# Kernel optimization log

Hardware: AMD Instinct MI355X
Metric: run time of the kernel (lower is better)

The kernel has to match this reference:

```python
import jax, jax.numpy as jnp
import numpy as np

B, C, H, W = 4, 256, 64, 64
EPS = 1e-5

def conv1x1(x, w, b):
    # x: [B,Cin,H,W], w: [Cout,Cin], b: [Cout]
    return jnp.einsum('bchw,oc->bohw', x, w) + b[None, :, None, None]

def setup_inputs() -> dict:
    key = jax.random.key(0)
    ks = jax.random.split(key, 16)
    s = 1.0 / np.sqrt(C)
    d = {
        'x1': jax.random.normal(ks[0], (B, C, H, W), jnp.float32),
        'x2': jax.random.normal(ks[1], (B, C, H, W), jnp.float32),
        'q_w': jax.random.normal(ks[2], (C, C), jnp.float32) * s,
        'q_b': jnp.zeros((C,), jnp.float32),
        'k_w': jax.random.normal(ks[3], (C, C), jnp.float32) * s,
        'k_b': jnp.zeros((C,), jnp.float32),
        'v_w': jax.random.normal(ks[4], (C, C), jnp.float32) * s,
        'v_b': jnp.zeros((C,), jnp.float32),
        'proj_w': jax.random.normal(ks[5], (C, C), jnp.float32) * s,
        'proj_b': jnp.zeros((C,), jnp.float32),
        'bn_gamma': jnp.ones((C,), jnp.float32),
        'bn_beta': jnp.zeros((C,), jnp.float32),
        'bn_mean': jax.random.normal(ks[6], (C,), jnp.float32) * 0.1,
        'bn_var': jax.random.uniform(ks[7], (C,), jnp.float32, 0.5, 1.5),
        'gate_w': jax.random.normal(ks[8], (1, 2 * C), jnp.float32) * (1.0 / np.sqrt(2 * C)),
        'gate_b': jnp.zeros((1,), jnp.float32),
    }
    return d

def reference(x1, x2, q_w, q_b, k_w, k_b, v_w, v_b, proj_w, proj_b,
              bn_gamma, bn_beta, bn_mean, bn_var, gate_w, gate_b):
    b, c, h, w = x1.shape
    n = h * w
    scale = c ** (-0.5)
    q = conv1x1(x1, q_w, q_b).reshape(b, c, n)   # [B,C,N]
    k = conv1x1(x2, k_w, k_b).reshape(b, c, n)
    v = conv1x1(x2, v_w, v_b).reshape(b, c, n)
    attn = jnp.einsum('bcn,bcm->bnm', q, k) * scale      # [B,N,N]
    attn = jax.nn.softmax(attn, axis=-1)
    fusion = jnp.einsum('bcm,bnm->bcn', v, attn)          # v @ attn^T
    fusion = fusion.reshape(b, c, h, w)
    # proj: conv1x1 -> BN (eval, running stats) -> ReLU
    fusion = conv1x1(fusion, proj_w, proj_b)
    fusion = (fusion - bn_mean[None, :, None, None]) * (
        bn_gamma[None, :, None, None] * jax.lax.rsqrt(bn_var + EPS)[None, :, None, None]
    ) + bn_beta[None, :, None, None]
    fusion = jax.nn.relu(fusion)
    gate = jax.nn.sigmoid(conv1x1(jnp.concatenate([x1, x2], axis=1), gate_w, gate_b))  # [B,1,H,W]
    return x1 + gate * fusion
```

## Files before the change

### kernel.cpp

```cpp
#include <hip/hip_runtime.h>
#include <hip/hip_bf16.h>

#define NB   4
#define C    256
#define NPIX 4096
#define EPSV 1e-5f
#define K2   0.09016844f
#define MFIX 24.0f
#define KVB  32
#define NSPLIT 4
#define NKVS (NPIX / NSPLIT)
#define NSTEPS (NKVS / KVB)

typedef __bf16 bf16x8 __attribute__((ext_vector_type(8)));
typedef float  f32x4  __attribute__((ext_vector_type(4)));
typedef float  f32x16 __attribute__((ext_vector_type(16)));
typedef unsigned int u32x4 __attribute__((ext_vector_type(4)));
typedef __hip_bfloat16 bf16;

__device__ __forceinline__ void gload16(const void* g, void* l) {
    __builtin_amdgcn_global_load_lds(
        (const __attribute__((address_space(1))) void*)g,
        (__attribute__((address_space(3))) void*)l, 16, 0, 0);
}

__global__ __launch_bounds__(256) void k_transpose(
    const float* __restrict__ x1, const float* __restrict__ x2,
    const float* __restrict__ gate_w,
    const float* __restrict__ qw, const float* __restrict__ kw,
    const float* __restrict__ vw, const float* __restrict__ pw,
    bf16* __restrict__ xt1, bf16* __restrict__ xt2,
    float* __restrict__ gate_ws, bf16* __restrict__ wb)
{
    __shared__ float tile[64][65];
    const int t = threadIdx.x;
    const int z = blockIdx.z;

    if (z == 8) {
        const int sub = blockIdx.x * 4 + blockIdx.y;
        const int i0 = sub * 1024 + t * 4;
        bf16 t4[4];
#pragma unroll
        for (int j = 0; j < 4; ++j) {
            const int i = i0 + j;
            const int p = i >> 16, rem = i & 65535;
            const int o = rem >> 8, cp = rem & 255;
            const int c = cp ^ ((o & 7) << 3);
            const float* w = (p == 0) ? qw : (p == 1) ? kw : (p == 2) ? vw : pw;
            t4[j] = __float2bfloat16(w[o * 256 + c]);
        }
        *reinterpret_cast<uint64_t*>(wb + i0) = *reinterpret_cast<uint64_t*>(t4);
        return;
    }

    const int nt = blockIdx.x, ct = blockIdx.y;
    const int b = z >> 1, which = z & 1;
    const float* x = which ? x2 : x1;
    bf16* xt = which ? xt2 : xt1;
    const int n0 = nt * 64, c0 = ct * 64;

    const float* xp = x + ((size_t)b * C + c0) * NPIX + n0;
#pragma unroll
    for (int i = 0; i < 16; ++i) {
        int cl = (t >> 6) + i * 4, nl = t & 63;
        tile[cl][nl] = xp[(size_t)cl * NPIX + nl];
    }
    __syncthreads();

    {
        int nl = t & 63, qq = t >> 6;
        float s = 0.f;
#pragma unroll
        for (int i = 0; i < 16; ++i) {
            int cl = qq * 16 + i;
            s += tile[cl][nl] * gate_w[which * C + c0 + cl];
        }
        atomicAdd(&gate_ws[b * NPIX + n0 + nl], s);
    }

    bf16* xtp = xt + ((size_t)b * NPIX + n0) * C + c0;
#pragma unroll
    for (int i = 0; i < 16; ++i) {
        int nl = (t >> 6) + i * 4, cl = t & 63;
        xtp[(size_t)nl * C + cl] = __float2bfloat16(tile[cl][nl]);
    }
}

__global__ __launch_bounds__(256) void k_qkv(
    const bf16* __restrict__ xt1, const bf16* __restrict__ xt2,
    const bf16* __restrict__ wb,
    const float* __restrict__ qb, const float* __restrict__ kb,
    const float* __restrict__ vb,
    bf16* __restrict__ Qt, bf16* __restrict__ Kt, bf16* __restrict__ Vv)
{
    __shared__ __align__(16) char wl[32768];
    const int nblk = blockIdx.x, ot = blockIdx.y, zp = blockIdx.z;
    const int b = zp / 3, pidx = zp % 3;
    const bf16* xt = (pidx == 0) ? xt1 : xt2;
    const float* bias = (pidx == 0) ? qb : (pidx == 1) ? kb : vb;
    const int o0 = ot * 64;
    const int t = threadIdx.x;
    const int wave = t >> 6, lane = t & 63;
    const int g = lane >> 4, l15 = lane & 15;

    {
        const char* src = (const char*)(wb + ((size_t)pidx * C + o0) * C);
#pragma unroll
        for (int i = 0; i < 8; ++i) {
            const int L = i * 4096 + t * 16;
            gload16(src + L, wl + L);
        }
    }
    asm volatile("s_waitcnt vmcnt(0)" ::: "memory");
    __syncthreads();

    bf16x8 a[4][8];
#pragma unroll
    for (int ns = 0; ns < 4; ++ns) {
        const bf16* xrow = xt + ((size_t)b * NPIX + nblk * 256 + wave * 64 + ns * 16 + l15) * C;
#pragma unroll
        for (int cb = 0; cb < 8; ++cb)
            a[ns][cb] = *reinterpret_cast<const bf16x8*>(xrow + cb * 32 + 8 * g);
    }

#pragma unroll
    for (int os = 0; os < 4; ++os) {
        const int oo = o0 + os * 16;
        bf16x8 wf[8];
#pragma unroll
        for (int cb = 0; cb < 8; ++cb)
            wf[cb] = *reinterpret_cast<const bf16x8*>(
                wl + (os * 16 + l15) * 512 + ((cb * 64 + 16 * g) ^ ((l15 & 7) << 4)));

        f32x4 acc[4] = {{0,0,0,0},{0,0,0,0},{0,0,0,0},{0,0,0,0}};
#pragma unroll
        for (int cb = 0; cb < 8; ++cb) {
#pragma unroll
            for (int ns = 0; ns < 4; ++ns) {
                if (pidx < 2)
                    acc[ns] = __builtin_amdgcn_mfma_f32_16x16x32_bf16(a[ns][cb], wf[cb], acc[ns], 0, 0, 0);
                else
                    acc[ns] = __builtin_amdgcn_mfma_f32_16x16x32_bf16(wf[cb], a[ns][cb], acc[ns], 0, 0, 0);
            }
        }

        if (pidx < 2) {
            const float bv = bias[oo + l15];
            const float scl = (pidx == 0) ? K2 : 1.0f;
            bf16* Qk = (pidx == 0) ? Qt : Kt;
#pragma unroll
            for (int ns = 0; ns < 4; ++ns) {
                const int n0 = nblk * 256 + wave * 64 + ns * 16;
                bf16* dst = Qk + ((size_t)b * NPIX + n0 + 4 * g) * C + oo + l15;
#pragma unroll
                for (int r = 0; r < 4; ++r)
                    dst[(size_t)r * C] = __float2bfloat16((acc[ns][r] + bv) * scl);
            }
        } else {
#pragma unroll
            for (int ns = 0; ns < 4; ++ns) {
                const int n0 = nblk * 256 + wave * 64 + ns * 16;
                bf16* dst = Vv + ((size_t)b * C + oo + 4 * g) * NPIX + n0 + l15;
#pragma unroll
                for (int r = 0; r < 4; ++r)
                    dst[(size_t)r * NPIX] = __float2bfloat16(acc[ns][r] + bias[oo + 4 * g + r]);
            }
        }
    }
}

#define SMEM_ATTN 65536
#define SZP ((size_t)NPIX * C)

__global__ __launch_bounds__(256, 2) void k_attn(
    const bf16* __restrict__ Qt, const bf16* __restrict__ Kt,
    const bf16* __restrict__ Vv, bf16* __restrict__ O0,
    bf16* __restrict__ O1, float2* __restrict__ mlws)
{
    extern __shared__ __align__(16) char smem[];
    const int id = blockIdx.x;
    const int combo = id & 15, nt = id >> 4;
    const int b = combo >> 2, split = combo & 3;
    const int m_base = split * NKVS;
    const int tid = threadIdx.x;
    const int wave = tid >> 6, lane = tid & 63;
    const int dl = lane & 31, hi = lane >> 5;
    const int n0 = nt * 128 + wave * 32;

    const bf16* Kg = Kt + (size_t)b * NPIX * C;
    const bf16* Vg = Vv + (size_t)b * C * NPIX;

    int o_k[4], o_v[4];
#pragma unroll
    for (int p = 0; p < 4; ++p) {
        const int L = p * 4096 + tid * 16;
        const int kv = L >> 9, colx = L & 511;
        const int col = colx ^ ((kv & 7) << 4);
        o_k[p] = kv * C + (col >> 1);
        const int R = L >> 7, colx2 = L & 127;
        const int col2 = colx2 ^ (((L >> 8) & 7) << 4);
        const int d = 2 * R + (col2 >> 6);
        o_v[p] = d * NPIX + ((col2 & 63) >> 1);
    }

    bf16x8 q[16];
    const bf16* qrow = Qt + ((size_t)b * NPIX + n0 + dl) * C + 8 * hi;
#pragma unroll
    for (int cs = 0; cs < 16; ++cs)
        q[cs] = *reinterpret_cast<const bf16x8*>(qrow + cs * 16);

    const int kRow = dl * 512, kmask = (lane & 7) << 4;
    const int vRow = (dl >> 1) * 128;
    const int vc0  = (((dl & 1) << 6) | (16 * hi)) ^ (((dl >> 2) & 7) << 4);

    f32x16 o[8];
#pragma unroll
    for (int i = 0; i < 8; ++i)
#pragma unroll
        for (int j = 0; j < 16; ++j) o[i][j] = 0.f;
    float m_run = MFIX, l_run = 0.f;

    auto stage = [&](int buf, int m0) {
        char* kd = smem + buf * 16384;
        char* vd = smem + 32768 + buf * 16384;
#pragma unroll
        for (int p = 0; p < 4; ++p) {
            gload16(Kg + (size_t)m0 * C + o_k[p], kd + p * 4096 + tid * 16);
            gload16(Vg + o_v[p] + m0,            vd + p * 4096 + tid * 16);
        }
    };

    stage(0, m_base);
    asm volatile("s_waitcnt vmcnt(0)" ::: "memory");
    __syncthreads();

    for (int t = 0; t < NSTEPS; ++t) {
        const int buf = t & 1;
        if (t + 1 < NSTEPS) stage(buf ^ 1, m_base + (t + 1) * KVB);

        const char* Kl = smem + buf * 16384;
        const char* Vl = smem + 32768 + buf * 16384;

        f32x16 s;
#pragma unroll
        for (int j = 0; j < 16; ++j) s[j] = 0.f;
        __builtin_amdgcn_s_setprio(1);
#pragma unroll
        for (int cs = 0; cs < 16; ++cs) {
            bf16x8 kf = *reinterpret_cast<const bf16x8*>(
                Kl + kRow + ((cs * 32 + 16 * hi) ^ kmask));
            s = __builtin_amdgcn_mfma_f32_32x32x16_bf16(kf, q[cs], s, 0, 0, 0);
        }
        __builtin_amdgcn_s_setprio(0);

        float m0v = fmaxf(s[0], s[1]),  m1v = fmaxf(s[2], s[3]);
        float m2v = fmaxf(s[4], s[5]),  m3v = fmaxf(s[6], s[7]);
        float m4v = fmaxf(s[8], s[9]),  m5v = fmaxf(s[10], s[11]);
        float m6v = fmaxf(s[12], s[13]), m7v = fmaxf(s[14], s[15]);
        float mx = fmaxf(fmaxf(fmaxf(m0v, m1v), fmaxf(m2v, m3v)),
                         fmaxf(fmaxf(m4v, m5v), fmaxf(m6v, m7v)));
        if (!__all(mx <= m_run)) {
            float mxr = fmaxf(mx, __shfl_xor(mx, 32));
            float mnew = fmaxf(m_run, mxr);
            float cf = exp2f(m_run - mnew);
            m_run = mnew;
            l_run *= cf;
#pragma unroll
            for (int i = 0; i < 8; ++i)
#pragma unroll
                for (int j = 0; j < 16; ++j) o[i][j] *= cf;
        }

        float psum = 0.f;
#pragma unroll
        for (int j = 0; j < 16; ++j) {
            s[j] = exp2f(s[j] - m_run);
            psum += s[j];
        }
        psum += __shfl_xor(psum, 32);
        l_run += psum;

        unsigned w[8];
#pragma unroll
        for (int i = 0; i < 8; ++i) {
            asm("v_cvt_pk_bf16_f32 %0, %1, %2"
                : "=v"(w[i]) : "v"(s[2 * i]), "v"(s[2 * i + 1]));
        }
        asm("v_permlane32_swap_b32 %0, %1" : "+v"(w[0]), "+v"(w[2]));
        asm("v_permlane32_swap_b32 %0, %1" : "+v"(w[1]), "+v"(w[3]));
        asm("v_permlane32_swap_b32 %0, %1" : "+v"(w[4]), "+v"(w[6]));
        asm("v_permlane32_swap_b32 %0, %1" : "+v"(w[5]), "+v"(w[7]));
        const bf16x8 pb0 = __builtin_bit_cast(bf16x8, (u32x4){w[0], w[1], w[2], w[3]});
        const bf16x8 pb1 = __builtin_bit_cast(bf16x8, (u32x4){w[4], w[5], w[6], w[7]});

        __builtin_amdgcn_s_setprio(1);
#pragma unroll
        for (int dt = 0; dt < 8; ++dt) {
            bf16x8 vf0 = *reinterpret_cast<const bf16x8*>(Vl + dt * 2048 + vRow + vc0);
            o[dt] = __builtin_amdgcn_mfma_f32_32x32x16_bf16(vf0, pb0, o[dt], 0, 0, 0);
            bf16x8 vf1 = *reinterpret_cast<const bf16x8*>(Vl + dt * 2048 + vRow + (vc0 ^ 32));
            o[dt] = __builtin_amdgcn_mfma_f32_32x32x16_bf16(vf1, pb1, o[dt], 0, 0, 0);
        }
        __builtin_amdgcn_s_setprio(0);

        asm volatile("s_waitcnt vmcnt(0)" ::: "memory");
        __syncthreads();
    }

    const int pp = split * NB + b;
    bf16* base = (pp < 8) ? (O0 + (size_t)pp * SZP) : (O1 + (size_t)(pp - 8) * SZP);
    const float invl = 1.0f / l_run;
    bf16* orow = base + (size_t)(n0 + dl) * C;
#pragma unroll
    for (int dt = 0; dt < 8; ++dt) {
#pragma unroll
        for (int a = 0; a < 4; ++a) {
            bf16 t4[4];
#pragma unroll
            for (int r = 0; r < 4; ++r)
                t4[r] = __float2bfloat16(o[dt][4 * a + r] * invl);
            *reinterpret_cast<uint64_t*>(orow + dt * 32 + 8 * a + 4 * hi) =
                *reinterpret_cast<uint64_t*>(t4);
        }
    }
    if (lane < 32)
        mlws[(size_t)pp * NPIX + n0 + dl] = make_float2(m_run, l_run);
}

__global__ __launch_bounds__(256) void k_combine(
    const bf16* __restrict__ O0, const bf16* __restrict__ O1,
    const float2* __restrict__ ml, bf16* __restrict__ Ot)
{
    const int tid = blockIdx.x * 256 + threadIdx.x;
    const int c8 = tid & 31;
    const int rest = tid >> 5;
    const int n = rest & 4095;
    const int b = rest >> 12;

    float2 a[NSPLIT];
#pragma unroll
    for (int s = 0; s < NSPLIT; ++s)
        a[s] = ml[(size_t)(s * NB + b) * NPIX + n];
    float M = fmaxf(fmaxf(a[0].x, a[1].x), fmaxf(a[2].x, a[3].x));
    float w[NSPLIT], tot = 0.f;
#pragma unroll
    for (int s = 0; s < NSPLIT; ++s) { w[s] = exp2f(a[s].x - M) * a[s].y; tot += w[s]; }
    float rs = 1.0f / tot;
#pragma unroll
    for (int s = 0; s < NSPLIT; ++s) w[s] *= rs;

    const size_t off = (size_t)n * C + c8 * 8;
    float acc[8] = {0,0,0,0,0,0,0,0};
#pragma unroll
    for (int s = 0; s < NSPLIT; ++s) {
        const int pp = s * NB + b;
        const bf16* src = ((pp < 8) ? (O0 + (size_t)pp * SZP)
                                    : (O1 + (size_t)(pp - 8) * SZP)) + off;
        bf16x8 x = *reinterpret_cast<const bf16x8*>(src);
#pragma unroll
        for (int j = 0; j < 8; ++j) acc[j] += w[s] * (float)x[j];
    }
    bf16 outv[8];
#pragma unroll
    for (int j = 0; j < 8; ++j) outv[j] = __float2bfloat16(acc[j]);
    *reinterpret_cast<bf16x8*>(Ot + ((size_t)b * NPIX + n) * C + c8 * 8) =
        *reinterpret_cast<bf16x8*>(outv);
}

__global__ __launch_bounds__(256) void k_proj(
    const bf16* __restrict__ Ot, const bf16* __restrict__ wb,
    const float* __restrict__ pb, const float* __restrict__ bn_g,
    const float* __restrict__ bn_b, const float* __restrict__ bn_m,
    const float* __restrict__ bn_v, const float* __restrict__ gate_ws,
    const float* __restrict__ gate_b, const float* __restrict__ x1,
    float* __restrict__ out)
{
    __shared__ __align__(16) char wl[32768];
    const int nblk = blockIdx.x, ot = blockIdx.y, b = blockIdx.z;
    const int o0 = ot * 64;
    const int t = threadIdx.x;
    const int wave = t >> 6, lane = t & 63;
    const int g = lane >> 4, l15 = lane & 15;

    {
        const char* src = (const char*)(wb + ((size_t)3 * C + o0) * C);
#pragma unroll
        for (int i = 0; i < 8; ++i) {
            const int L = i * 4096 + t * 16;
            gload16(src + L, wl + L);
        }
    }
    asm volatile("s_waitcnt vmcnt(0)" ::: "memory");
    __syncthreads();

    bf16x8 bfr[2][8];
#pragma unroll
    for (int ns = 0; ns < 2; ++ns) {
        const bf16* orow = Ot + ((size_t)b * NPIX + nblk * 128 + wave * 32 + ns * 16 + l15) * C;
#pragma unroll
        for (int cb = 0; cb < 8; ++cb)
            bfr[ns][cb] = *reinterpret_cast<const bf16x8*>(orow + cb * 32 + 8 * g);
    }
    const float gb = gate_b[0];

#pragma unroll
    for (int os = 0; os < 4; ++os) {
        const int oo = o0 + os * 16;
        bf16x8 wf[8];
#pragma unroll
        for (int cb = 0; cb < 8; ++cb)
            wf[cb] = *reinterpret_cast<const bf16x8*>(
                wl + (os * 16 + l15) * 512 + ((cb * 64 + 16 * g) ^ ((l15 & 7) << 4)));

        f32x4 acc[2] = {{0,0,0,0},{0,0,0,0}};
#pragma unroll
        for (int cb = 0; cb < 8; ++cb) {
            acc[0] = __builtin_amdgcn_mfma_f32_16x16x32_bf16(wf[cb], bfr[0][cb], acc[0], 0, 0, 0);
            acc[1] = __builtin_amdgcn_mfma_f32_16x16x32_bf16(wf[cb], bfr[1][cb], acc[1], 0, 0, 0);
        }

#pragma unroll
        for (int ns = 0; ns < 2; ++ns) {
            const int n0 = nblk * 128 + wave * 32 + ns * 16;
            float gsum = gate_ws[b * NPIX + n0 + l15];
            float gate = 1.f / (1.f + __expf(-(gsum + gb)));
#pragma unroll
            for (int r = 0; r < 4; ++r) {
                int oc = oo + 4 * g + r;
                float scl = bn_g[oc] * rsqrtf(bn_v[oc] + EPSV);
                float v = (acc[ns][r] + pb[oc] - bn_m[oc]) * scl + bn_b[oc];
                v = fmaxf(v, 0.f);
                size_t idx = ((size_t)b * C + oc) * NPIX + n0 + l15;
                out[idx] = x1[idx] + gate * v;
            }
        }
    }
}

extern "C" void kernel_launch(void* const* d_in, const int* in_sizes, int n_in,
                              void* d_out, int out_size, void* d_ws, size_t ws_size,
                              hipStream_t stream)
{
    const float* x1  = (const float*)d_in[0];
    const float* x2  = (const float*)d_in[1];
    const float* q_w = (const float*)d_in[2];
    const float* q_b = (const float*)d_in[3];
    const float* k_w = (const float*)d_in[4];
    const float* k_b = (const float*)d_in[5];
    const float* v_w = (const float*)d_in[6];
    const float* v_b = (const float*)d_in[7];
    const float* p_w = (const float*)d_in[8];
    const float* p_b = (const float*)d_in[9];
    const float* bn_g = (const float*)d_in[10];
    const float* bn_b = (const float*)d_in[11];
    const float* bn_m = (const float*)d_in[12];
    const float* bn_v = (const float*)d_in[13];
    const float* g_w  = (const float*)d_in[14];
    const float* g_b  = (const float*)d_in[15];
    float* out = (float*)d_out;

    const size_t szBF = (size_t)NB * NPIX * C * sizeof(bf16);
    char* p = (char*)d_ws;
    bf16* xt1 = (bf16*)p; p += szBF;
    bf16* xt2 = (bf16*)p; p += szBF;
    bf16* Qt  = (bf16*)p; p += szBF;
    bf16* Kt  = (bf16*)p; p += szBF;
    bf16* Vv  = (bf16*)p; p += szBF;
    float* gate_ws = (float*)p; p += (size_t)NB * NPIX * sizeof(float);
    float2* mlws = (float2*)p; p += (size_t)16 * NPIX * sizeof(float2);
    bf16* wb = (bf16*)p;

    bf16* O0 = (bf16*)d_out;
    bf16* O1 = xt1;
    bf16* Ot = Qt;

    hipFuncSetAttribute((const void*)k_attn,
                        hipFuncAttributeMaxDynamicSharedMemorySize, SMEM_ATTN);

    hipMemsetAsync(gate_ws, 0, (size_t)NB * NPIX * sizeof(float), stream);
    k_transpose<<<dim3(64, 4, 9),  256, 0, stream>>>(x1, x2, g_w, q_w, k_w, v_w, p_w,
                                                     xt1, xt2, gate_ws, wb);
    k_qkv     <<<dim3(16, 4, 12), 256, 0, stream>>>(xt1, xt2, wb, q_b, k_b, v_b,
                                                    Qt, Kt, Vv);
    k_attn    <<<dim3(512), 256, SMEM_ATTN, stream>>>(Qt, Kt, Vv, O0, O1, mlws);
    k_combine <<<dim3(2048), 256, 0, stream>>>(O0, O1, mlws, Ot);
    k_proj    <<<dim3(32, 4, 4),  256, 0, stream>>>(Ot, wb, p_b, bn_g, bn_b, bn_m,
                                                    bn_v, gate_ws, g_b, x1, out);
}
```

Baseline: 157.2 us.

## Store Q and K in FP8 and compute attention scores with FP8 MFMA

The QKV projection now writes Q and K as FP8 e4m3 bytes instead of bf16, and the attention kernel computes the QK^T scores with the 32x32x16 fp8 MFMA. This halves K tile staging and shared memory (48KB instead of 64KB), with a new swizzle for the narrower rows. Q register fragments shrink from 16 bf16x8 vectors to 16 longs, and global traffic for Q and K drops. The cost is reduced score precision, since Q and K are quantised to e4m3 with no per-tensor scaling. This could push softmax error past tolerance.

```diff
diff --git a/kernel.cpp b/kernel.cpp
--- a/kernel.cpp
+++ b/kernel.cpp
@@ -1,5 +1,6 @@
 #include <hip/hip_runtime.h>
 #include <hip/hip_bf16.h>
+#include <hip/hip_fp8.h>
 
 #define NB   4
 #define C    256
@@ -22,6 +23,10 @@
     __builtin_amdgcn_global_load_lds(
         (const __attribute__((address_space(1))) void*)g,
         (__attribute__((address_space(3))) void*)l, 16, 0, 0);
+}
+
+__device__ __forceinline__ unsigned char to_fp8(float x) {
+    return __hip_fp8_e4m3(x).__x;
 }
 
 __global__ __launch_bounds__(256) void k_transpose(
@@ -91,7 +96,8 @@
     const bf16* __restrict__ wb,
     const float* __restrict__ qb, const float* __restrict__ kb,
     const float* __restrict__ vb,
-    bf16* __restrict__ Qt, bf16* __restrict__ Kt, bf16* __restrict__ Vv)
+    unsigned char* __restrict__ Qt, unsigned char* __restrict__ Kt,
+    bf16* __restrict__ Vv)
 {
     __shared__ __align__(16) char wl[32768];
     const int nblk = blockIdx.x, ot = blockIdx.y, zp = blockIdx.z;
@@ -147,14 +153,14 @@
         if (pidx < 2) {
             const float bv = bias[oo + l15];
             const float scl = (pidx == 0) ? K2 : 1.0f;
-            bf16* Qk = (pidx == 0) ? Qt : Kt;
+            unsigned char* Qk = (pidx == 0) ? Qt : Kt;
 #pragma unroll
             for (int ns = 0; ns < 4; ++ns) {
                 const int n0 = nblk * 256 + wave * 64 + ns * 16;
-                bf16* dst = Qk + ((size_t)b * NPIX + n0 + 4 * g) * C + oo + l15;
+                unsigned char* dst = Qk + ((size_t)b * NPIX + n0 + 4 * g) * C + oo + l15;
 #pragma unroll
                 for (int r = 0; r < 4; ++r)
-                    dst[(size_t)r * C] = __float2bfloat16((acc[ns][r] + bv) * scl);
+                    dst[(size_t)r * C] = to_fp8((acc[ns][r] + bv) * scl);
             }
         } else {
 #pragma unroll
@@ -169,11 +175,11 @@
     }
 }
 
-#define SMEM_ATTN 65536
+#define SMEM_ATTN 49152
 #define SZP ((size_t)NPIX * C)
 
 __global__ __launch_bounds__(256, 2) void k_attn(
-    const bf16* __restrict__ Qt, const bf16* __restrict__ Kt,
+    const unsigned char* __restrict__ Qt, const unsigned char* __restrict__ Kt,
     const bf16* __restrict__ Vv, bf16* __restrict__ O0,
     bf16* __restrict__ O1, float2* __restrict__ mlws)
 {
@@ -187,29 +193,33 @@
     const int dl = lane & 31, hi = lane >> 5;
     const int n0 = nt * 128 + wave * 32;
 
-    const bf16* Kg = Kt + (size_t)b * NPIX * C;
+    const unsigned char* Kg = Kt + (size_t)b * NPIX * C;
     const bf16* Vg = Vv + (size_t)b * C * NPIX;
 
-    int o_k[4], o_v[4];
+    int o_k[2], o_v[4];
+#pragma unroll
+    for (int p = 0; p < 2; ++p) {
+        const int L = p * 4096 + tid * 16;
+        const int kv = L >> 8;
+        const int col = (L & 255) ^ ((kv & 15) << 4);
+        o_k[p] = kv * C + col;
+    }
 #pragma unroll
     for (int p = 0; p < 4; ++p) {
         const int L = p * 4096 + tid * 16;
-        const int kv = L >> 9, colx = L & 511;
-        const int col = colx ^ ((kv & 7) << 4);
-        o_k[p] = kv * C + (col >> 1);
         const int R = L >> 7, colx2 = L & 127;
         const int col2 = colx2 ^ (((L >> 8) & 7) << 4);
         const int d = 2 * R + (col2 >> 6);
         o_v[p] = d * NPIX + ((col2 & 63) >> 1);
     }
 
-    bf16x8 q[16];
-    const bf16* qrow = Qt + ((size_t)b * NPIX + n0 + dl) * C + 8 * hi;
+    long q[16];
+    const unsigned char* qrow = Qt + ((size_t)b * NPIX + n0 + dl) * C + 8 * hi;
 #pragma unroll
     for (int cs = 0; cs < 16; ++cs)
-        q[cs] = *reinterpret_cast<const bf16x8*>(qrow + cs * 16);
-
-    const int kRow = dl * 512, kmask = (lane & 7) << 4;
+        q[cs] = *reinterpret_cast<const long*>(qrow + cs * 16);
+
+    const int kRow = dl * 256, kmask = (dl & 15) << 4;
     const int vRow = (dl >> 1) * 128;
     const int vc0  = (((dl & 1) << 6) | (16 * hi)) ^ (((dl >> 2) & 7) << 4);
 
@@ -221,13 +231,14 @@
     float m_run = MFIX, l_run = 0.f;
 
     auto stage = [&](int buf, int m0) {
-        char* kd = smem + buf * 16384;
-        char* vd = smem + 32768 + buf * 16384;
-#pragma unroll
-        for (int p = 0; p < 4; ++p) {
+        char* kd = smem + buf * 24576;
+        char* vd = kd + 8192;
+#pragma unroll
+        for (int p = 0; p < 2; ++p)
             gload16(Kg + (size_t)m0 * C + o_k[p], kd + p * 4096 + tid * 16);
-            gload16(Vg + o_v[p] + m0,            vd + p * 4096 + tid * 16);
-        }
+#pragma unroll
+        for (int p = 0; p < 4; ++p)
+            gload16(Vg + o_v[p] + m0, vd + p * 4096 + tid * 16);
     };
 
     stage(0, m_base);
@@ -238,8 +249,8 @@
         const int buf = t & 1;
         if (t + 1 < NSTEPS) stage(buf ^ 1, m_base + (t + 1) * KVB);
 
-        const char* Kl = smem + buf * 16384;
-        const char* Vl = smem + 32768 + buf * 16384;
+        const char* Kl = smem + buf * 24576;
+        const char* Vl = Kl + 8192;
 
         f32x16 s;
 #pragma unroll
@@ -247,9 +258,9 @@
         __builtin_amdgcn_s_setprio(1);
 #pragma unroll
         for (int cs = 0; cs < 16; ++cs) {
-            bf16x8 kf = *reinterpret_cast<const bf16x8*>(
-                Kl + kRow + ((cs * 32 + 16 * hi) ^ kmask));
-            s = __builtin_amdgcn_mfma_f32_32x32x16_bf16(kf, q[cs], s, 0, 0, 0);
+            long kf = *reinterpret_cast<const long*>(
+                Kl + kRow + ((cs * 16 + 8 * hi) ^ kmask));
+            s = __builtin_amdgcn_mfma_f32_32x32x16_fp8_fp8(kf, q[cs], s, 0, 0, 0);
         }
         __builtin_amdgcn_s_setprio(0);
 
@@ -463,16 +474,19 @@
     char* p = (char*)d_ws;
     bf16* xt1 = (bf16*)p; p += szBF;
     bf16* xt2 = (bf16*)p; p += szBF;
-    bf16* Qt  = (bf16*)p; p += szBF;
-    bf16* Kt  = (bf16*)p; p += szBF;
+    char* QtS = p; p += szBF;
+    char* KtS = p; p += szBF;
     bf16* Vv  = (bf16*)p; p += szBF;
     float* gate_ws = (float*)p; p += (size_t)NB * NPIX * sizeof(float);
     float2* mlws = (float2*)p; p += (size_t)16 * NPIX * sizeof(float2);
     bf16* wb = (bf16*)p;
 
+    unsigned char* Qt8 = (unsigned char*)QtS;
+    unsigned char* Kt8 = (unsigned char*)KtS;
+
     bf16* O0 = (bf16*)d_out;
     bf16* O1 = xt1;
-    bf16* Ot = Qt;
+    bf16* Ot = (bf16*)QtS;
 
     hipFuncSetAttribute((const void*)k_attn,
                         hipFuncAttributeMaxDynamicSharedMemorySize, SMEM_ATTN);
@@ -481,8 +495,8 @@
     k_transpose<<<dim3(64, 4, 9),  256, 0, stream>>>(x1, x2, g_w, q_w, k_w, v_w, p_w,
                                                      xt1, xt2, gate_ws, wb);
     k_qkv     <<<dim3(16, 4, 12), 256, 0, stream>>>(xt1, xt2, wb, q_b, k_b, v_b,
-                                                    Qt, Kt, Vv);
-    k_attn    <<<dim3(512), 256, SMEM_ATTN, stream>>>(Qt, Kt, Vv, O0, O1, mlws);
+                                                    Qt8, Kt8, Vv);
+    k_attn    <<<dim3(512), 256, SMEM_ATTN, stream>>>(Qt8, Kt8, Vv, O0, O1, mlws);
     k_combine <<<dim3(2048), 256, 0, stream>>>(O0, O1, mlws, Ot);
     k_proj    <<<dim3(32, 4, 4),  256, 0, stream>>>(Ot, wb, p_b, bn_g, bn_b, bn_m,
                                                     bn_v, gate_ws, g_b, x1, out);
```

Result: faster. 144.5 us (-8.1%).
